# Optimization experiments

Measured on AMD Instinct MI355X. Metric: run time of the kernel, lower is better.

Reference implementation:

```python
import jax, jax.numpy as jnp
import numpy as np

B, IN, H = 4096, 1024, 2048

def setup_inputs() -> dict:
    key = jax.random.key(0)
    ks = jax.random.split(key, 7)
    sk = (1.0 / H) ** 0.5
    return {
        "x": jax.random.normal(ks[0], (B, IN), dtype=jnp.float32),
        "prev_h": jax.random.normal(ks[1], (B, H), dtype=jnp.float32),
        "prev_c": jax.random.normal(ks[2], (B, H), dtype=jnp.float32),
        "W_i": jax.random.uniform(ks[3], (H, H + IN), dtype=jnp.float32, minval=-sk, maxval=sk),
        "W_f": jax.random.uniform(ks[4], (H, H + IN), dtype=jnp.float32, minval=-sk, maxval=sk),
        "W_o": jax.random.uniform(ks[5], (H, H + IN), dtype=jnp.float32, minval=-sk, maxval=sk),
        "W_c": jax.random.uniform(ks[6], (H, H + IN), dtype=jnp.float32, minval=-sk, maxval=sk),
    }

def reference(x, prev_h, prev_c, W_i, W_f, W_o, W_c):
    # concat (h, x) along features: [B, H+IN]
    hx = jnp.concatenate([prev_h, x], axis=1)
    # stack 4 gate weights -> single GEMM: [B, H+IN] @ [H+IN, 4H]
    W = jnp.concatenate([W_i, W_f, W_o, W_c], axis=0)  # [4H, H+IN]
    gates = hx @ W.T  # [B, 4H]
    gi, gf, go, gc = jnp.split(gates, 4, axis=1)
    i = jax.nn.sigmoid(gi)
    f = jax.nn.sigmoid(gf)
    o = jax.nn.sigmoid(go)
    c_tilde = jnp.tanh(gc)
    next_c = f * prev_c + i * c_tilde
    next_h = o * jnp.tanh(next_c)
    return next_h, next_c
```

## Files before the change

### kernel.cpp

```cpp
#include <hip/hip_runtime.h>
#include <hip/hip_bf16.h>


#define BATCH 4096
#define INW   1024
#define HID   2048
#define GK    3072
#define GN    8192

typedef __attribute__((ext_vector_type(8))) short short8;
typedef __attribute__((ext_vector_type(4))) float floatx4;

__device__ __forceinline__ unsigned short f2bf(float f) {
    union { float f; unsigned u; } v; v.f = f;
    unsigned r = v.u + 0x7FFFu + ((v.u >> 16) & 1u);
    return (unsigned short)(r >> 16);
}
__device__ __forceinline__ float bf2f(unsigned short u) {
    union { unsigned u; float f; } v; v.u = ((unsigned)u) << 16;
    return v.f;
}
__device__ __forceinline__ float sigf(float x) {
    return 1.0f / (1.0f + __expf(-x));
}
__device__ __forceinline__ float tanhfast(float x) {
    float t = __expf(fminf(fmaxf(2.0f * x, -30.0f), 30.0f));
    return (t - 1.0f) / (t + 1.0f);
}

__global__ __launch_bounds__(256) void pack_all(const float4* __restrict__ ph,
                                                const float4* __restrict__ x,
                                                const float4* __restrict__ Wi,
                                                const float4* __restrict__ Wf,
                                                const float4* __restrict__ Wo,
                                                const float4* __restrict__ Wc,
                                                unsigned short* __restrict__ hx,
                                                unsigned short* __restrict__ Wb) {
    long i = (long)blockIdx.x * 256 + threadIdx.x;
    const float4* src;
    unsigned short* dst;
    if (i < 1048576L) {
        int r  = (int)(i >> 8);
        int c8 = (int)(i & 255);
        src = ph + 2 * i;
        dst = hx + (size_t)r * GK + (size_t)c8 * 8;
    } else if (i < 1572864L) {
        long j = i - 1048576L;
        int r  = (int)(j >> 7);
        int c8 = (int)(j & 127);
        src = x + 2 * j;
        dst = hx + (size_t)r * GK + HID + (size_t)c8 * 8;
    } else {
        long j = i - 1572864L;
        const float4* Wg;
        int g;
        if (j < 786432L)            { Wg = Wi; g = 0; }
        else if (j < 1572864L)      { Wg = Wf; g = 1; j -= 786432L; }
        else if (j < 2359296L)      { Wg = Wo; g = 2; j -= 1572864L; }
        else                        { Wg = Wc; g = 3; j -= 2359296L; }
        src = Wg + 2 * j;
        dst = Wb + (size_t)g * HID * GK + (size_t)j * 8;
    }
    float4 v0 = src[0];
    float4 v1 = src[1];
    unsigned short o[8];
    o[0] = f2bf(v0.x); o[1] = f2bf(v0.y); o[2] = f2bf(v0.z); o[3] = f2bf(v0.w);
    o[4] = f2bf(v1.x); o[5] = f2bf(v1.y); o[6] = f2bf(v1.z); o[7] = f2bf(v1.w);
    *(short8*)dst = *(const short8*)o;
}

__device__ __forceinline__ void gld16(const unsigned short* g, unsigned short* l) {
    __builtin_amdgcn_global_load_lds((const __attribute__((address_space(1))) unsigned int*)g,
                                     (__attribute__((address_space(3))) unsigned int*)l,
                                     16, 0, 0);
}

__global__ __launch_bounds__(256) void gemm_bt(const unsigned short* __restrict__ A,
                                               const unsigned short* __restrict__ Bt,
                                               unsigned short* __restrict__ C) {
    __shared__ unsigned short lA[128 * 64];
    __shared__ unsigned short lB[128 * 64];
    const int tid  = threadIdx.x;
    const int wave = tid >> 6;
    const int lane = tid & 63;
    const long row0 = (long)blockIdx.x * 128;
    const long col0 = (long)blockIdx.y * 128;

    const int r_loc = tid >> 3;
    const int c0    = ((tid & 7) - r_loc) & 7;

    const unsigned short* gA[4];
    const unsigned short* gB[4];
    #pragma unroll
    for (int j = 0; j < 4; j++) {
        gA[j] = A  + (row0 + j * 32 + r_loc) * GK + c0 * 8;
        gB[j] = Bt + (col0 + j * 32 + r_loc) * GK + c0 * 8;
    }
    unsigned short* lAs = &lA[tid * 8];
    unsigned short* lBs = &lB[tid * 8];

    floatx4 acc[4][4];
    #pragma unroll
    for (int mi = 0; mi < 4; mi++)
        #pragma unroll
        for (int ni = 0; ni < 4; ni++)
            acc[mi][ni] = (floatx4)(0.0f);

    const int mBase = (wave >> 1) << 6;
    const int nBase = (wave & 1) << 6;
    const int fr = lane & 15;
    const int cq = lane >> 4;

    for (int k0 = 0; k0 < GK; k0 += 64) {
        __syncthreads();
        #pragma unroll
        for (int j = 0; j < 4; j++) gld16(gA[j] + k0, lAs + j * 2048);
        #pragma unroll
        for (int j = 0; j < 4; j++) gld16(gB[j] + k0, lBs + j * 2048);
        __syncthreads();

        #pragma unroll
        for (int ks = 0; ks < 2; ks++) {
            const int ci = ks * 4 + cq;
            short8 af[4], bfv[4];
            #pragma unroll
            for (int mi = 0; mi < 4; mi++) {
                int R = mBase + mi * 16 + fr;
                af[mi] = *(const short8*)&lA[R * 64 + (((ci + R) & 7) << 3)];
            }
            #pragma unroll
            for (int ni = 0; ni < 4; ni++) {
                int R = nBase + ni * 16 + fr;
                bfv[ni] = *(const short8*)&lB[R * 64 + (((ci + R) & 7) << 3)];
            }
            #pragma unroll
            for (int mi = 0; mi < 4; mi++)
                #pragma unroll
                for (int ni = 0; ni < 4; ni++)
                    acc[mi][ni] = __builtin_amdgcn_mfma_f32_16x16x32_bf16(af[mi], bfv[ni], acc[mi][ni], 0, 0, 0);
        }
    }

    const int cr = (lane >> 4) << 2;
    const int cc = lane & 15;
    #pragma unroll
    for (int mi = 0; mi < 4; mi++) {
        #pragma unroll
        for (int ni = 0; ni < 4; ni++) {
            long base = (row0 + mBase + mi * 16 + cr) * (long)GN + col0 + nBase + ni * 16 + cc;
            #pragma unroll
            for (int r = 0; r < 4; r++)
                C[base + (long)r * GN] = f2bf(acc[mi][ni][r]);
        }
    }
}

__global__ __launch_bounds__(256) void lstm_ep(const unsigned short* __restrict__ gates,
                                               const float* __restrict__ prev_c,
                                               float* __restrict__ out) {
    const int i = blockIdx.x * 256 + threadIdx.x;
    const int b = i >> 9;
    const int h = (i & 511) << 2;
    const size_t gb = (size_t)b * GN + h;
    ushort4 gi = *(const ushort4*)&gates[gb];
    ushort4 gf = *(const ushort4*)&gates[gb + HID];
    ushort4 go = *(const ushort4*)&gates[gb + 2 * HID];
    ushort4 gc = *(const ushort4*)&gates[gb + 3 * HID];
    const size_t ob = (size_t)b * HID + h;
    float4 c4 = *(const float4*)&prev_c[ob];

    unsigned short giv[4] = {gi.x, gi.y, gi.z, gi.w};
    unsigned short gfv[4] = {gf.x, gf.y, gf.z, gf.w};
    unsigned short gov[4] = {go.x, go.y, go.z, go.w};
    unsigned short gcv[4] = {gc.x, gc.y, gc.z, gc.w};
    float cv[4] = {c4.x, c4.y, c4.z, c4.w};
    float nh[4], nc[4];
    #pragma unroll
    for (int j = 0; j < 4; j++) {
        float vi = sigf(bf2f(giv[j]));
        float vf = sigf(bf2f(gfv[j]));
        float vo = sigf(bf2f(gov[j]));
        float vc = tanhfast(bf2f(gcv[j]));
        float ncf = vf * cv[j] + vi * vc;
        float nhf = vo * tanhfast(ncf);
        nc[j] = ncf;
        nh[j] = nhf;
    }
    float4 vh = {nh[0], nh[1], nh[2], nh[3]};
    float4 vc4 = {nc[0], nc[1], nc[2], nc[3]};
    *(float4*)&out[ob] = vh;
    *(float4*)&out[(size_t)BATCH * HID + ob] = vc4;
}

extern "C" void kernel_launch(void* const* d_in, const int* in_sizes, int n_in,
                              void* d_out, int out_size, void* d_ws, size_t ws_size,
                              hipStream_t stream) {
    const float* x   = (const float*)d_in[0];
    const float* ph  = (const float*)d_in[1];
    const float* pc  = (const float*)d_in[2];
    const float* Wi  = (const float*)d_in[3];
    const float* Wf  = (const float*)d_in[4];
    const float* Wo  = (const float*)d_in[5];
    const float* Wc  = (const float*)d_in[6];

    unsigned short* hx    = (unsigned short*)d_ws;
    unsigned short* Wb    = hx + (size_t)BATCH * GK;
    unsigned short* gates = Wb + (size_t)GN * GK;
    float* out = (float*)d_out;

    pack_all<<<18432, 256, 0, stream>>>((const float4*)ph, (const float4*)x,
                                        (const float4*)Wi, (const float4*)Wf,
                                        (const float4*)Wo, (const float4*)Wc,
                                        hx, Wb);

    gemm_bt<<<dim3(BATCH / 128, GN / 128), 256, 0, stream>>>(hx, Wb, gates);

    lstm_ep<<<(BATCH * HID / 4) / 256, 256, 0, stream>>>(gates, pc, out);
}
```

Before: 412.7 us.

## Restructure GEMM into 256x256 tiles with 4-stage async LDS pipeline

Replaces the 128x128 single-buffered GEMM with 512-thread blocks computing 256x256 tiles over K-steps of 32. A 4-deep ring of LDS buffers is filled by async global-to-LDS loads issued three steps ahead, gated by explicit vmcnt waits. Each step is split into two half-phases with barriers and raised wave priority around the MFMA bursts. A block-index swizzle groups neighbouring tiles for L2 reuse. The aim is to hide global load latency behind the matrix-core work and raise arithmetic intensity, in exchange for more registers (128 accumulator floats per lane), 128 KB of LDS per block and hand-tuned synchronisation that is easy to get wrong.

```diff
diff --git a/kernel.cpp b/kernel.cpp
--- a/kernel.cpp
+++ b/kernel.cpp
@@ -75,82 +75,121 @@
                                      16, 0, 0);
 }
 
-__global__ __launch_bounds__(256) void gemm_bt(const unsigned short* __restrict__ A,
-                                               const unsigned short* __restrict__ Bt,
-                                               unsigned short* __restrict__ C) {
-    __shared__ unsigned short lA[128 * 64];
-    __shared__ unsigned short lB[128 * 64];
+template<int VM> __device__ __forceinline__ void wait_vm() {
+    if constexpr (VM == 8)      asm volatile("s_waitcnt vmcnt(8)" ::: "memory");
+    else if constexpr (VM == 4) asm volatile("s_waitcnt vmcnt(4)" ::: "memory");
+    else if constexpr (VM == 0) asm volatile("s_waitcnt vmcnt(0)" ::: "memory");
+}
+
+__global__ __launch_bounds__(512, 2) void gemm_bt(const unsigned short* __restrict__ A,
+                                                  const unsigned short* __restrict__ Bt,
+                                                  unsigned short* __restrict__ C) {
+    __shared__ unsigned short lds[65536];
     const int tid  = threadIdx.x;
     const int wave = tid >> 6;
     const int lane = tid & 63;
-    const long row0 = (long)blockIdx.x * 128;
-    const long col0 = (long)blockIdx.y * 128;
-
-    const int r_loc = tid >> 3;
-    const int c0    = ((tid & 7) - r_loc) & 7;
-
-    const unsigned short* gA[4];
-    const unsigned short* gB[4];
-    #pragma unroll
-    for (int j = 0; j < 4; j++) {
-        gA[j] = A  + (row0 + j * 32 + r_loc) * GK + c0 * 8;
-        gB[j] = Bt + (col0 + j * 32 + r_loc) * GK + c0 * 8;
-    }
-    unsigned short* lAs = &lA[tid * 8];
-    unsigned short* lBs = &lB[tid * 8];
-
-    floatx4 acc[4][4];
-    #pragma unroll
-    for (int mi = 0; mi < 4; mi++)
-        #pragma unroll
-        for (int ni = 0; ni < 4; ni++)
-            acc[mi][ni] = (floatx4)(0.0f);
-
-    const int mBase = (wave >> 1) << 6;
-    const int nBase = (wave & 1) << 6;
+
+    const int bid = blockIdx.x;
+    const int swz = ((bid & 7) << 6) + (bid >> 3);
+    const long row0 = (long)(swz >> 5) * 256;
+    const long col0 = (long)(swz & 31) * 256;
+
+    const int wm = wave >> 2;
+    const int wn = wave & 3;
+
+    const int c0 = ((tid & 3) - ((tid >> 3) & 3)) & 3;
+    const unsigned short* gA0 = A  + (row0 + (tid >> 2)) * GK + c0 * 8;
+    const unsigned short* gB0 = Bt + (col0 + (tid >> 2)) * GK + c0 * 8;
+
+#define STAGE_A(kt, b) do { \
+        unsigned short* _d = &lds[(b) * 8192 + tid * 8]; \
+        gld16(gA0 + (size_t)(kt) * 32, _d); \
+        gld16(gA0 + 128 * GK + (size_t)(kt) * 32, _d + 4096); \
+    } while (0)
+#define STAGE_B(kt, b) do { \
+        unsigned short* _d = &lds[32768 + (b) * 8192 + tid * 8]; \
+        gld16(gB0 + (size_t)(kt) * 32, _d); \
+        gld16(gB0 + 128 * GK + (size_t)(kt) * 32, _d + 4096); \
+    } while (0)
+
     const int fr = lane & 15;
     const int cq = lane >> 4;
-
-    for (int k0 = 0; k0 < GK; k0 += 64) {
-        __syncthreads();
+    const int slot = ((cq + (fr >> 1)) & 3) << 3;
+    const int aoff = (wm * 128 + fr) * 32 + slot;
+    const int boff = (wn * 64 + fr) * 32 + slot;
+
+    floatx4 acc[8][4];
+    #pragma unroll
+    for (int i = 0; i < 8; i++)
         #pragma unroll
-        for (int j = 0; j < 4; j++) gld16(gA[j] + k0, lAs + j * 2048);
-        #pragma unroll
-        for (int j = 0; j < 4; j++) gld16(gB[j] + k0, lBs + j * 2048);
-        __syncthreads();
-
-        #pragma unroll
-        for (int ks = 0; ks < 2; ks++) {
-            const int ci = ks * 4 + cq;
-            short8 af[4], bfv[4];
-            #pragma unroll
-            for (int mi = 0; mi < 4; mi++) {
-                int R = mBase + mi * 16 + fr;
-                af[mi] = *(const short8*)&lA[R * 64 + (((ci + R) & 7) << 3)];
-            }
-            #pragma unroll
-            for (int ni = 0; ni < 4; ni++) {
-                int R = nBase + ni * 16 + fr;
-                bfv[ni] = *(const short8*)&lB[R * 64 + (((ci + R) & 7) << 3)];
-            }
-            #pragma unroll
-            for (int mi = 0; mi < 4; mi++)
-                #pragma unroll
-                for (int ni = 0; ni < 4; ni++)
-                    acc[mi][ni] = __builtin_amdgcn_mfma_f32_16x16x32_bf16(af[mi], bfv[ni], acc[mi][ni], 0, 0, 0);
-        }
-    }
+        for (int j = 0; j < 4; j++)
+            acc[i][j] = (floatx4)(0.0f);
+
+    STAGE_A(0, 0); STAGE_B(0, 0);
+    STAGE_A(1, 1); STAGE_B(1, 1);
+    STAGE_A(2, 2); STAGE_B(2, 2);
+    asm volatile("s_waitcnt vmcnt(8)" ::: "memory");
+    __builtin_amdgcn_s_barrier();
+
+#define K_ITER(t, VMW, STG) do { \
+        const unsigned short* bufA = &lds[((t) & 3) * 8192]; \
+        const unsigned short* bufB = &lds[32768 + ((t) & 3) * 8192]; \
+        short8 af[4], bfv[4]; \
+         \
+        _Pragma("unroll") \
+        for (int i = 0; i < 4; i++) af[i]  = *(const short8*)&bufA[aoff + i * 512]; \
+        _Pragma("unroll") \
+        for (int j = 0; j < 4; j++) bfv[j] = *(const short8*)&bufB[boff + j * 512]; \
+        if (STG) { STAGE_A((t) + 3, ((t) + 3) & 3); } \
+        __builtin_amdgcn_s_barrier(); \
+        asm volatile("s_waitcnt lgkmcnt(0)" ::: "memory"); \
+        __builtin_amdgcn_sched_barrier(0); \
+        __builtin_amdgcn_s_setprio(1); \
+        _Pragma("unroll") \
+        for (int i = 0; i < 4; i++) \
+            _Pragma("unroll") \
+            for (int j = 0; j < 4; j++) \
+                acc[i][j] = __builtin_amdgcn_mfma_f32_16x16x32_bf16(af[i], bfv[j], acc[i][j], 0, 0, 0); \
+        __builtin_amdgcn_s_setprio(0); \
+        __builtin_amdgcn_s_barrier(); \
+         \
+        _Pragma("unroll") \
+        for (int i = 0; i < 4; i++) af[i] = *(const short8*)&bufA[aoff + 2048 + i * 512]; \
+        if (STG) { STAGE_B((t) + 3, ((t) + 3) & 3); } \
+        __builtin_amdgcn_s_barrier(); \
+        asm volatile("s_waitcnt lgkmcnt(0)" ::: "memory"); \
+        __builtin_amdgcn_sched_barrier(0); \
+        __builtin_amdgcn_s_setprio(1); \
+        _Pragma("unroll") \
+        for (int i = 0; i < 4; i++) \
+            _Pragma("unroll") \
+            for (int j = 0; j < 4; j++) \
+                acc[4 + i][j] = __builtin_amdgcn_mfma_f32_16x16x32_bf16(af[i], bfv[j], acc[4 + i][j], 0, 0, 0); \
+        __builtin_amdgcn_s_setprio(0); \
+        wait_vm<VMW>(); \
+        __builtin_amdgcn_s_barrier(); \
+    } while (0)
+
+    int t = 0;
+    for (; t < 93; ++t) K_ITER(t, 8, true);
+    K_ITER(93, 4, false);
+    K_ITER(94, 0, false);
+    K_ITER(95, -1, false);
+
+#undef K_ITER
+#undef STAGE_A
+#undef STAGE_B
 
     const int cr = (lane >> 4) << 2;
     const int cc = lane & 15;
     #pragma unroll
-    for (int mi = 0; mi < 4; mi++) {
+    for (int mi = 0; mi < 8; mi++) {
         #pragma unroll
-        for (int ni = 0; ni < 4; ni++) {
-            long base = (row0 + mBase + mi * 16 + cr) * (long)GN + col0 + nBase + ni * 16 + cc;
+        for (int nj = 0; nj < 4; nj++) {
+            long base = (row0 + wm * 128 + mi * 16 + cr) * (long)GN + col0 + wn * 64 + nj * 16 + cc;
             #pragma unroll
             for (int r = 0; r < 4; r++)
-                C[base + (long)r * GN] = f2bf(acc[mi][ni][r]);
+                C[base + (long)r * GN] = f2bf(acc[mi][nj][r]);
         }
     }
 }
@@ -213,7 +252,7 @@
                                         (const float4*)Wo, (const float4*)Wc,
                                         hx, Wb);
 
-    gemm_bt<<<dim3(BATCH / 128, GN / 128), 256, 0, stream>>>(hx, Wb, gates);
+    gemm_bt<<<512, 512, 0, stream>>>(hx, Wb, gates);
 
     lstm_ep<<<(BATCH * HID / 4) / 256, 256, 0, stream>>>(gates, pc, out);
 }
```

New measurement: 408.2 us. No clear change (-1.1%).
